# Performance work log

Measured on AMD Instinct MI355X. Metric: run time of the kernel, lower is better.

The kernel has to match this reference:

```python
import jax, jax.numpy as jnp
import numpy as np

N = 50000        # nodes
E = 1600000      # edges (avg degree 32)
N_IN = 128       # atomic embedding dim
N_F = 128        # filter dim
N_G = 50         # gaussian basis size for fij
CUTOFF = 5.0


def setup_inputs() -> dict:
    key = jax.random.key(0)
    ks = jax.random.split(key, 12)
    feat = jax.random.normal(ks[0], (N, N_IN), jnp.float32)
    fij = jax.random.uniform(ks[1], (E, N_G), dtype=jnp.float32)
    rij = jax.random.uniform(ks[2], (E,), dtype=jnp.float32) * CUTOFF
    src = jax.random.randint(ks[3], (E,), 0, N, dtype=jnp.int32)
    dst = jax.random.randint(ks[4], (E,), 0, N, dtype=jnp.int32)

    def w(k, shape, fan_in):
        return jax.random.normal(k, shape, jnp.float32) / np.float32(np.sqrt(fan_in))

    W_in2f = w(ks[5], (N_IN, N_F), N_IN)                 # Dense(n_in, n_filters, bias=False)
    Wf1 = w(ks[6], (N_G, N_F), N_G); bf1 = jnp.zeros((N_F,), jnp.float32)   # filter_network layer 1 (swish)
    Wf2 = w(ks[7], (N_F, N_F), N_F); bf2 = jnp.zeros((N_F,), jnp.float32)   # filter_network layer 2
    Wm1 = w(ks[8], (N_F, N_IN), N_F); bm1 = jnp.zeros((N_IN,), jnp.float32) # msg_transform layer 1 (swish)
    Wm2 = w(ks[9], (N_IN, N_IN), N_IN); bm2 = jnp.zeros((N_IN,), jnp.float32)
    return dict(feat=feat, fij=fij, rij=rij, src=src, dst=dst,
                W_in2f=W_in2f, Wf1=Wf1, bf1=bf1, Wf2=Wf2, bf2=bf2,
                Wm1=Wm1, bm1=bm1, Wm2=Wm2, bm2=bm2)


def _swish(x):
    return x * jax.nn.sigmoid(x)


def reference(feat, fij, rij, src, dst, W_in2f, Wf1, bf1, Wf2, bf2, Wm1, bm1, Wm2, bm2):
    # Cosine cutoff: 0.5*(cos(pi*r/rc)+1) for r < rc, else 0
    C = 0.5 * (jnp.cos(jnp.pi * rij / CUTOFF) + 1.0) * (rij < CUTOFF).astype(rij.dtype)
    # Edge filters: filter_network(fij) * C  -> [E, n_filters]
    he = (_swish(fij @ Wf1 + bf1) @ Wf2 + bf2) * C[:, None]
    # Node features projected: in2f(feat) -> [N, n_filters]
    hv = feat @ W_in2f
    # u_mul_e: gather source node feature, multiply by edge filter -> [E, n_filters]
    m = hv[src] * he
    # aggregator: sum messages at destination nodes -> [N, n_filters]
    agg = jax.ops.segment_sum(m, dst, num_segments=N)
    # msg_transform: Dense(swish) -> Dense
    return _swish(agg @ Wm1 + bm1) @ Wm2 + bm2
```

## Files before the change

### kernel.cpp

```cpp
#include <hip/hip_runtime.h>

#define N_NODES 50000
#define N_EDGES 1600000

typedef _Float16 f16x8 __attribute__((ext_vector_type(8)));
typedef float f32x4 __attribute__((ext_vector_type(4)));

__device__ __forceinline__ float fast_rcp(float v) {
#if __has_builtin(__builtin_amdgcn_rcpf)
    return __builtin_amdgcn_rcpf(v);
#else
    return __frcp_rn(v);
#endif
}

__global__ void prep_weights(const float* __restrict__ Wf1,
                             const float* __restrict__ Wf2,
                             const float* __restrict__ W_in2f,
                             const float* __restrict__ Wm1,
                             const float* __restrict__ Wm2,
                             _Float16* __restrict__ W1img,
                             _Float16* __restrict__ W2img,
                             _Float16* __restrict__ Wi2fimg,
                             _Float16* __restrict__ Wm1img,
                             _Float16* __restrict__ Wm2img) {
    int i = blockIdx.x * 256 + threadIdx.x;
    if (i < 8192) {
        int n = i >> 6, k = i & 63;
        float v = (k < 50) ? Wf1[k * 128 + n] : 0.0f;
        W1img[n * 64 + (((k >> 3) ^ (n & 7)) << 3) + (k & 7)] = (_Float16)v;
    }
    if (i < 16384) {
        int n = i >> 7, k = i & 127;
        int off = n * 128 + (((k >> 3) ^ (n & 7)) << 3) + (k & 7);
        int src = k * 128 + n;
        W2img[off]   = (_Float16)Wf2[src];
        Wi2fimg[off] = (_Float16)W_in2f[src];
        Wm1img[off]  = (_Float16)Wm1[src];
        Wm2img[off]  = (_Float16)Wm2[src];
    }
}

__global__ __launch_bounds__(512) void fused_hv_hist(
        const float* __restrict__ feat, const _Float16* __restrict__ Wi2fimg,
        _Float16* __restrict__ hvh,
        const int* __restrict__ dstv, int* __restrict__ cnt) {
    const int b = blockIdx.x;
    const int tid = threadIdx.x;
    if (b < 391) {
        const int lane = tid & 63, wv = tid >> 6;
        const int l15 = lane & 15, q = lane >> 4;
        const int row0 = b * 128;
        int ar = row0 + wv * 16 + l15;
        if (ar > N_NODES - 1) ar = N_NODES - 1;
        const float* arow = feat + (long)ar * 128;
        f16x8 a[4];
        #pragma unroll
        for (int ks = 0; ks < 4; ++ks) {
            const float* p = arow + ks * 32 + q * 8;
            float2 u0 = *(const float2*)(p + 0);
            float2 u1 = *(const float2*)(p + 2);
            float2 u2 = *(const float2*)(p + 4);
            float2 u3 = *(const float2*)(p + 6);
            a[ks][0] = (_Float16)u0.x; a[ks][1] = (_Float16)u0.y;
            a[ks][2] = (_Float16)u1.x; a[ks][3] = (_Float16)u1.y;
            a[ks][4] = (_Float16)u2.x; a[ks][5] = (_Float16)u2.y;
            a[ks][6] = (_Float16)u3.x; a[ks][7] = (_Float16)u3.y;
        }
        f32x4 acc[8];
        for (int nb = 0; nb < 8; ++nb) acc[nb] = (f32x4){0.f, 0.f, 0.f, 0.f};
        #pragma unroll
        for (int ks = 0; ks < 4; ++ks) {
            int c = ks * 4 + q;
            #pragma unroll
            for (int nb = 0; nb < 8; ++nb) {
                int n = nb * 16 + l15;
                f16x8 bf = *(const f16x8*)&Wi2fimg[n * 128 + ((c ^ (n & 7)) << 3)];
                acc[nb] = __builtin_amdgcn_mfma_f32_16x16x32_f16(a[ks], bf, acc[nb], 0, 0, 0);
            }
        }
        #pragma unroll
        for (int nb = 0; nb < 8; ++nb)
            #pragma unroll
            for (int r = 0; r < 4; ++r) {
                int orow = row0 + wv * 16 + q * 4 + r;
                if (orow < N_NODES)
                    hvh[(long)orow * 128 + nb * 16 + l15] = (_Float16)acc[nb][r];
            }
    } else {
        int e = (b - 391) * 512 + tid;
        if (e < N_EDGES) atomicAdd(&cnt[dstv[e]], 1);
    }
}

__global__ __launch_bounds__(1024) void scan_reduce(const int* __restrict__ cnt,
                                                    int* __restrict__ bsum) {
    __shared__ int ws[16];
    int tid = threadIdx.x, lane = tid & 63;
    int i = blockIdx.x * 1024 + tid;
    int x = (i < N_NODES) ? cnt[i] : 0;
    for (int o = 32; o > 0; o >>= 1) x += __shfl_down(x, o);
    if (lane == 0) ws[tid >> 6] = x;
    __syncthreads();
    if (tid == 0) {
        int s = 0;
        for (int w = 0; w < 16; ++w) s += ws[w];
        bsum[blockIdx.x] = s;
    }
}

__global__ void scan_top(int* __restrict__ bsum) {
    if (threadIdx.x == 0) {
        int s = 0;
        for (int b = 0; b < 49; ++b) { int v = bsum[b]; bsum[b] = s; s += v; }
    }
}

__global__ __launch_bounds__(1024) void scan_apply(int* __restrict__ cnt,
                                                   const int* __restrict__ bsum) {
    __shared__ int ws[16], wo[16];
    int tid = threadIdx.x, lane = tid & 63, wid = tid >> 6;
    int i = blockIdx.x * 1024 + tid;
    int x = (i < N_NODES) ? cnt[i] : 0;
    int incl = x;
    for (int o = 1; o < 64; o <<= 1) {
        int y = __shfl_up(incl, o);
        if (lane >= o) incl += y;
    }
    if (lane == 63) ws[wid] = incl;
    __syncthreads();
    if (tid == 0) {
        int s = 0;
        for (int w = 0; w < 16; ++w) { wo[w] = s; s += ws[w]; }
    }
    __syncthreads();
    if (i < N_NODES) cnt[i] = bsum[blockIdx.x] + wo[wid] + incl - x;
}

__global__ void scatter_kernel(const int* __restrict__ dstv,
                               const int* __restrict__ srcv,
                               const float* __restrict__ rij,
                               int* __restrict__ cursor,
                               int4* __restrict__ meta) {
    int e = blockIdx.x * 256 + threadIdx.x;
    if (e < N_EDGES) {
        int d = dstv[e];
        int pos = atomicAdd(&cursor[d], 1);
        meta[pos] = make_int4(e, srcv[e], d, __float_as_int(rij[e]));
    }
}

__global__ __launch_bounds__(512, 4) void edge_kernel(
        const float* __restrict__ fij, const _Float16* __restrict__ hvh,
        const _Float16* __restrict__ W1img, const _Float16* __restrict__ W2img,
        const float* __restrict__ bf1, const float* __restrict__ bf2,
        const int4* __restrict__ meta, float* __restrict__ agg) {
    __shared__ __align__(16) char smem[65536];
    __shared__ __align__(16) int4 sMeta[128];
    _Float16* sW1 = (_Float16*)smem;
    _Float16* sW2 = (_Float16*)(smem + 16384);
    _Float16* sT0 = (_Float16*)smem;
    _Float16* sT1 = (_Float16*)(smem + 49152);
    _Float16* sM  = (_Float16*)(smem + 16384);

    const int tid = threadIdx.x;
    const int lane = tid & 63;
    const int wv = tid >> 6;
    const int l15 = lane & 15;
    const int q = lane >> 4;
    const int e0 = blockIdx.x * 128;

    const int arow = wv * 16 + l15;
    const int eid = meta[e0 + arow].x;
    const float* frow = fij + (long)eid * 50;
    float2 p0 = *(const float2*)(frow + q * 8 + 0);
    float2 p1 = *(const float2*)(frow + q * 8 + 2);
    float2 p2 = *(const float2*)(frow + q * 8 + 4);
    float2 p3 = *(const float2*)(frow + q * 8 + 6);
    const int kb = 32 + q * 8;
    float2 z2 = make_float2(0.f, 0.f);
    float2 p4 = (kb + 1 < 50) ? *(const float2*)(frow + kb + 0) : z2;
    float2 p5 = (kb + 3 < 50) ? *(const float2*)(frow + kb + 2) : z2;
    float2 p6 = (kb + 5 < 50) ? *(const float2*)(frow + kb + 4) : z2;
    float2 p7 = (kb + 7 < 50) ? *(const float2*)(frow + kb + 6) : z2;
    f16x8 a0, a1;
    a0[0] = (_Float16)p0.x; a0[1] = (_Float16)p0.y;
    a0[2] = (_Float16)p1.x; a0[3] = (_Float16)p1.y;
    a0[4] = (_Float16)p2.x; a0[5] = (_Float16)p2.y;
    a0[6] = (_Float16)p3.x; a0[7] = (_Float16)p3.y;
    a1[0] = (_Float16)p4.x; a1[1] = (_Float16)p4.y;
    a1[2] = (_Float16)p5.x; a1[3] = (_Float16)p5.y;
    a1[4] = (_Float16)p6.x; a1[5] = (_Float16)p6.y;
    a1[6] = (_Float16)p7.x; a1[7] = (_Float16)p7.y;

    if (tid < 128) sMeta[tid] = meta[e0 + tid];
    {
        const float4* s1 = (const float4*)W1img;
        float4* d1 = (float4*)sW1;
        d1[tid] = s1[tid]; d1[tid + 512] = s1[tid + 512];
        const float4* s2 = (const float4*)W2img;
        float4* d2 = (float4*)sW2;
        for (int t = 0; t < 4; ++t) d2[tid + 512 * t] = s2[tid + 512 * t];
    }
    float b1v[8], b2v[8];
    for (int nb = 0; nb < 8; ++nb) {
        b1v[nb] = bf1[nb * 16 + l15];
        b2v[nb] = bf2[nb * 16 + l15];
    }
    __syncthreads();

    const int col2 = tid & 63;
    const int rseg0 = (tid >> 6) * 16;
    unsigned int pf[16];
    #pragma unroll
    for (int i = 0; i < 16; ++i) {
        long srcn = sMeta[rseg0 + i].y;
        pf[i] = *(const unsigned int*)(hvh + srcn * 128 + col2 * 2);
    }

    f32x4 acc[8];
    for (int nb = 0; nb < 8; ++nb) acc[nb] = (f32x4){0.f, 0.f, 0.f, 0.f};
    {
        f16x8 b[8];
        for (int nb = 0; nb < 8; ++nb) {
            int n = nb * 16 + l15;
            b[nb] = *(const f16x8*)&sW1[n * 64 + ((q ^ (n & 7)) << 3)];
        }
        for (int nb = 0; nb < 8; ++nb)
            acc[nb] = __builtin_amdgcn_mfma_f32_16x16x32_f16(a0, b[nb], acc[nb], 0, 0, 0);
        for (int nb = 0; nb < 8; ++nb) {
            int n = nb * 16 + l15;
            b[nb] = *(const f16x8*)&sW1[n * 64 + (((4 + q) ^ (n & 7)) << 3)];
        }
        for (int nb = 0; nb < 8; ++nb)
            acc[nb] = __builtin_amdgcn_mfma_f32_16x16x32_f16(a1, b[nb], acc[nb], 0, 0, 0);
    }
    __syncthreads();

    for (int nb = 0; nb < 8; ++nb)
        for (int r = 0; r < 4; ++r) {
            float x = acc[nb][r] + b1v[nb];
            float tt = x * fast_rcp(1.0f + __expf(-x));
            int row = wv * 16 + q * 4 + r;
            int col = nb * 16 + l15;
            _Float16* base = (row < 64) ? sT0 + row * 128 : sT1 + (row - 64) * 128;
            base[(((col >> 3) ^ (row & 7)) << 3) + (col & 7)] = (_Float16)tt;
        }
    __syncthreads();

    for (int nb = 0; nb < 8; ++nb) acc[nb] = (f32x4){0.f, 0.f, 0.f, 0.f};
    {
        const int row = wv * 16 + l15;
        const _Float16* abase = (row < 64) ? sT0 + row * 128 : sT1 + (row - 64) * 128;
        for (int ks = 0; ks < 4; ++ks) {
            int c = ks * 4 + q;
            f16x8 a = *(const f16x8*)&abase[(c ^ (row & 7)) << 3];
            for (int nb = 0; nb < 8; ++nb) {
                int n = nb * 16 + l15;
                f16x8 b = *(const f16x8*)&sW2[n * 128 + ((c ^ (n & 7)) << 3)];
                acc[nb] = __builtin_amdgcn_mfma_f32_16x16x32_f16(a, b, acc[nb], 0, 0, 0);
            }
        }
    }
    __syncthreads();

    for (int r = 0; r < 4; ++r) {
        int row = wv * 16 + q * 4 + r;
        float rv = __int_as_float(sMeta[row].w);
        float Cr = (rv < 5.0f) ? 0.5f * (__cosf(0.6283185307179586f * rv) + 1.0f) : 0.0f;
        for (int nb = 0; nb < 8; ++nb) {
            int col = nb * 16 + l15;
            sM[row * 132 + col] = (_Float16)((acc[nb][r] + b2v[nb]) * Cr);
        }
    }
    __syncthreads();

    {
        float run0 = 0.0f, run1 = 0.0f;
        int cur = sMeta[rseg0].z;
        #pragma unroll
        for (int i = 0; i < 16; ++i) {
            int r = rseg0 + i;
            int d = sMeta[r].z;
            if (d != cur) {
                atomicAdd(&agg[cur * 128 + col2 * 2], run0);
                atomicAdd(&agg[cur * 128 + col2 * 2 + 1], run1);
                run0 = 0.0f; run1 = 0.0f; cur = d;
            }
            union { unsigned int u; _Float16 h[2]; } hv2; hv2.u = pf[i];
            union { unsigned int u; _Float16 h[2]; } m2;
            m2.u = *(const unsigned int*)&sM[r * 132 + col2 * 2];
            run0 += (float)hv2.h[0] * (float)m2.h[0];
            run1 += (float)hv2.h[1] * (float)m2.h[1];
        }
        atomicAdd(&agg[cur * 128 + col2 * 2], run0);
        atomicAdd(&agg[cur * 128 + col2 * 2 + 1], run1);
    }
}

__global__ __launch_bounds__(512) void out_kernel(const float* __restrict__ agg,
                                                  const _Float16* __restrict__ Wm1img,
                                                  const float* __restrict__ bm1,
                                                  const _Float16* __restrict__ Wm2img,
                                                  const float* __restrict__ bm2,
                                                  float* __restrict__ out) {
    __shared__ __align__(16) _Float16 sT[128 * 128];
    const int tid = threadIdx.x, lane = tid & 63, wv = tid >> 6;
    const int l15 = lane & 15, q = lane >> 4;
    const int row0 = blockIdx.x * 128;
    int ar = row0 + wv * 16 + l15;
    if (ar > N_NODES - 1) ar = N_NODES - 1;
    const float* arow = agg + (long)ar * 128;
    f16x8 a[4];
    #pragma unroll
    for (int ks = 0; ks < 4; ++ks) {
        const float* p = arow + ks * 32 + q * 8;
        float2 u0 = *(const float2*)(p + 0);
        float2 u1 = *(const float2*)(p + 2);
        float2 u2 = *(const float2*)(p + 4);
        float2 u3 = *(const float2*)(p + 6);
        a[ks][0] = (_Float16)u0.x; a[ks][1] = (_Float16)u0.y;
        a[ks][2] = (_Float16)u1.x; a[ks][3] = (_Float16)u1.y;
        a[ks][4] = (_Float16)u2.x; a[ks][5] = (_Float16)u2.y;
        a[ks][6] = (_Float16)u3.x; a[ks][7] = (_Float16)u3.y;
    }
    float b1v[8], b2v[8];
    for (int nb = 0; nb < 8; ++nb) {
        b1v[nb] = bm1[nb * 16 + l15];
        b2v[nb] = bm2[nb * 16 + l15];
    }
    f32x4 acc[8];
    for (int nb = 0; nb < 8; ++nb) acc[nb] = (f32x4){0.f, 0.f, 0.f, 0.f};
    #pragma unroll
    for (int ks = 0; ks < 4; ++ks) {
        int c = ks * 4 + q;
        #pragma unroll
        for (int nb = 0; nb < 8; ++nb) {
            int n = nb * 16 + l15;
            f16x8 bf = *(const f16x8*)&Wm1img[n * 128 + ((c ^ (n & 7)) << 3)];
            acc[nb] = __builtin_amdgcn_mfma_f32_16x16x32_f16(a[ks], bf, acc[nb], 0, 0, 0);
        }
    }
    #pragma unroll
    for (int nb = 0; nb < 8; ++nb)
        #pragma unroll
        for (int r = 0; r < 4; ++r) {
            float x = acc[nb][r] + b1v[nb];
            float tt = x * fast_rcp(1.0f + __expf(-x));
            int row = wv * 16 + q * 4 + r;
            int col = nb * 16 + l15;
            sT[row * 128 + (((col >> 3) ^ (row & 7)) << 3) + (col & 7)] = (_Float16)tt;
        }
    __syncthreads();
    for (int nb = 0; nb < 8; ++nb) acc[nb] = (f32x4){0.f, 0.f, 0.f, 0.f};
    {
        const int rowA = wv * 16 + l15;
        const _Float16* abase = &sT[rowA * 128];
        #pragma unroll
        for (int ks = 0; ks < 4; ++ks) {
            int c = ks * 4 + q;
            f16x8 a2 = *(const f16x8*)&abase[(c ^ (rowA & 7)) << 3];
            #pragma unroll
            for (int nb = 0; nb < 8; ++nb) {
                int n = nb * 16 + l15;
                f16x8 bf = *(const f16x8*)&Wm2img[n * 128 + ((c ^ (n & 7)) << 3)];
                acc[nb] = __builtin_amdgcn_mfma_f32_16x16x32_f16(a2, bf, acc[nb], 0, 0, 0);
            }
        }
    }
    #pragma unroll
    for (int nb = 0; nb < 8; ++nb)
        #pragma unroll
        for (int r = 0; r < 4; ++r) {
            int orow = row0 + wv * 16 + q * 4 + r;
            if (orow < N_NODES)
                out[(long)orow * 128 + nb * 16 + l15] = acc[nb][r] + b2v[nb];
        }
}

extern "C" void kernel_launch(void* const* d_in, const int* in_sizes, int n_in,
                              void* d_out, int out_size, void* d_ws, size_t ws_size,
                              hipStream_t stream) {
    const float* feat   = (const float*)d_in[0];
    const float* fij    = (const float*)d_in[1];
    const float* rij    = (const float*)d_in[2];
    const int*   srcv   = (const int*)d_in[3];
    const int*   dstv   = (const int*)d_in[4];
    const float* W_in2f = (const float*)d_in[5];
    const float* Wf1    = (const float*)d_in[6];
    const float* bf1    = (const float*)d_in[7];
    const float* Wf2    = (const float*)d_in[8];
    const float* bf2    = (const float*)d_in[9];
    const float* Wm1    = (const float*)d_in[10];
    const float* bm1    = (const float*)d_in[11];
    const float* Wm2    = (const float*)d_in[12];
    const float* bm2    = (const float*)d_in[13];
    float* out = (float*)d_out;

    char* ws = (char*)d_ws;
    float*    agg     = (float*)ws;
    _Float16* hvh     = (_Float16*)(ws + 25600000);
    int4*     meta    = (int4*)(ws + 38400000);
    int*      cnt     = (int*)(ws + 64000000);
    int*      bsum    = (int*)(ws + 64200000);
    _Float16* W1img   = (_Float16*)(ws + 64200704);
    _Float16* W2img   = (_Float16*)(ws + 64217088);
    _Float16* Wi2fimg = (_Float16*)(ws + 64249856);
    _Float16* Wm1img  = (_Float16*)(ws + 64282624);
    _Float16* Wm2img  = (_Float16*)(ws + 64315392);

    hipMemsetAsync(agg, 0, (size_t)N_NODES * 128 * sizeof(float), stream);
    hipMemsetAsync(cnt, 0, (size_t)N_NODES * sizeof(int), stream);
    prep_weights<<<64, 256, 0, stream>>>(Wf1, Wf2, W_in2f, Wm1, Wm2,
                                         W1img, W2img, Wi2fimg, Wm1img, Wm2img);
    fused_hv_hist<<<391 + 3125, 512, 0, stream>>>(feat, Wi2fimg, hvh, dstv, cnt);
    scan_reduce<<<49, 1024, 0, stream>>>(cnt, bsum);
    scan_top<<<1, 64, 0, stream>>>(bsum);
    scan_apply<<<49, 1024, 0, stream>>>(cnt, bsum);
    scatter_kernel<<<(N_EDGES + 255) / 256, 256, 0, stream>>>(dstv, srcv, rij, cnt, meta);
    edge_kernel<<<12500, 512, 0, stream>>>(fij, hvh, W1img, W2img, bf1, bf2, meta, agg);
    out_kernel<<<391, 512, 0, stream>>>(agg, Wm1img, bm1, Wm2img, bm2, out);
}
```

Before: 871.7 us.

## Read filter weights from global, make edge kernel wave-local and barrier-free

Weight tiles W1/W2 are no longer staged into shared memory. MFMA B fragments are loaded straight from the global weight images, relying on cache hits. Because each wave only touches its own 16 rows, the intermediate and message buffers are merged into one 32KB swizzled shared array and all block-wide barriers after setup are removed. Launch bounds are raised to request more resident blocks. The cost is much more cache traffic for weight fragments, and register pressure from the tighter occupancy target could cause spills.

```diff
diff --git a/kernel.cpp b/kernel.cpp
--- a/kernel.cpp
+++ b/kernel.cpp
@@ -150,18 +150,13 @@
     }
 }
 
-__global__ __launch_bounds__(512, 4) void edge_kernel(
+__global__ __launch_bounds__(512, 8) void edge_kernel(
         const float* __restrict__ fij, const _Float16* __restrict__ hvh,
         const _Float16* __restrict__ W1img, const _Float16* __restrict__ W2img,
         const float* __restrict__ bf1, const float* __restrict__ bf2,
         const int4* __restrict__ meta, float* __restrict__ agg) {
-    __shared__ __align__(16) char smem[65536];
+    __shared__ __align__(16) _Float16 sTM[128 * 128];
     __shared__ __align__(16) int4 sMeta[128];
-    _Float16* sW1 = (_Float16*)smem;
-    _Float16* sW2 = (_Float16*)(smem + 16384);
-    _Float16* sT0 = (_Float16*)smem;
-    _Float16* sT1 = (_Float16*)(smem + 49152);
-    _Float16* sM  = (_Float16*)(smem + 16384);
 
     const int tid = threadIdx.x;
     const int lane = tid & 63;
@@ -194,14 +189,6 @@
     a1[6] = (_Float16)p7.x; a1[7] = (_Float16)p7.y;
 
     if (tid < 128) sMeta[tid] = meta[e0 + tid];
-    {
-        const float4* s1 = (const float4*)W1img;
-        float4* d1 = (float4*)sW1;
-        d1[tid] = s1[tid]; d1[tid + 512] = s1[tid + 512];
-        const float4* s2 = (const float4*)W2img;
-        float4* d2 = (float4*)sW2;
-        for (int t = 0; t < 4; ++t) d2[tid + 512 * t] = s2[tid + 512 * t];
-    }
     float b1v[8], b2v[8];
     for (int nb = 0; nb < 8; ++nb) {
         b1v[nb] = bf1[nb * 16 + l15];
@@ -209,8 +196,23 @@
     }
     __syncthreads();
 
+    f32x4 acc[8];
+    for (int nb = 0; nb < 8; ++nb) acc[nb] = (f32x4){0.f, 0.f, 0.f, 0.f};
+    #pragma unroll
+    for (int nb = 0; nb < 8; ++nb) {
+        int n = nb * 16 + l15;
+        f16x8 b = *(const f16x8*)&W1img[n * 64 + ((q ^ (n & 7)) << 3)];
+        acc[nb] = __builtin_amdgcn_mfma_f32_16x16x32_f16(a0, b, acc[nb], 0, 0, 0);
+    }
+    #pragma unroll
+    for (int nb = 0; nb < 8; ++nb) {
+        int n = nb * 16 + l15;
+        f16x8 b = *(const f16x8*)&W1img[n * 64 + (((4 + q) ^ (n & 7)) << 3)];
+        acc[nb] = __builtin_amdgcn_mfma_f32_16x16x32_f16(a1, b, acc[nb], 0, 0, 0);
+    }
+
     const int col2 = tid & 63;
-    const int rseg0 = (tid >> 6) * 16;
+    const int rseg0 = wv * 16;
     unsigned int pf[16];
     #pragma unroll
     for (int i = 0; i < 16; ++i) {
@@ -218,62 +220,46 @@
         pf[i] = *(const unsigned int*)(hvh + srcn * 128 + col2 * 2);
     }
 
-    f32x4 acc[8];
-    for (int nb = 0; nb < 8; ++nb) acc[nb] = (f32x4){0.f, 0.f, 0.f, 0.f};
-    {
-        f16x8 b[8];
-        for (int nb = 0; nb < 8; ++nb) {
-            int n = nb * 16 + l15;
-            b[nb] = *(const f16x8*)&sW1[n * 64 + ((q ^ (n & 7)) << 3)];
-        }
-        for (int nb = 0; nb < 8; ++nb)
-            acc[nb] = __builtin_amdgcn_mfma_f32_16x16x32_f16(a0, b[nb], acc[nb], 0, 0, 0);
-        for (int nb = 0; nb < 8; ++nb) {
-            int n = nb * 16 + l15;
-            b[nb] = *(const f16x8*)&sW1[n * 64 + (((4 + q) ^ (n & 7)) << 3)];
-        }
-        for (int nb = 0; nb < 8; ++nb)
-            acc[nb] = __builtin_amdgcn_mfma_f32_16x16x32_f16(a1, b[nb], acc[nb], 0, 0, 0);
-    }
-    __syncthreads();
-
+    #pragma unroll
     for (int nb = 0; nb < 8; ++nb)
+        #pragma unroll
         for (int r = 0; r < 4; ++r) {
             float x = acc[nb][r] + b1v[nb];
             float tt = x * fast_rcp(1.0f + __expf(-x));
             int row = wv * 16 + q * 4 + r;
             int col = nb * 16 + l15;
-            _Float16* base = (row < 64) ? sT0 + row * 128 : sT1 + (row - 64) * 128;
-            base[(((col >> 3) ^ (row & 7)) << 3) + (col & 7)] = (_Float16)tt;
-        }
-    __syncthreads();
+            sTM[row * 128 + (((col >> 3) ^ (row & 7)) << 3) + (col & 7)] = (_Float16)tt;
+        }
 
     for (int nb = 0; nb < 8; ++nb) acc[nb] = (f32x4){0.f, 0.f, 0.f, 0.f};
     {
         const int row = wv * 16 + l15;
-        const _Float16* abase = (row < 64) ? sT0 + row * 128 : sT1 + (row - 64) * 128;
+        const _Float16* abase = &sTM[row * 128];
+        #pragma unroll
         for (int ks = 0; ks < 4; ++ks) {
             int c = ks * 4 + q;
             f16x8 a = *(const f16x8*)&abase[(c ^ (row & 7)) << 3];
+            #pragma unroll
             for (int nb = 0; nb < 8; ++nb) {
                 int n = nb * 16 + l15;
-                f16x8 b = *(const f16x8*)&sW2[n * 128 + ((c ^ (n & 7)) << 3)];
+                f16x8 b = *(const f16x8*)&W2img[n * 128 + ((c ^ (n & 7)) << 3)];
                 acc[nb] = __builtin_amdgcn_mfma_f32_16x16x32_f16(a, b, acc[nb], 0, 0, 0);
             }
         }
     }
-    __syncthreads();
-
+
+    #pragma unroll
     for (int r = 0; r < 4; ++r) {
         int row = wv * 16 + q * 4 + r;
         float rv = __int_as_float(sMeta[row].w);
         float Cr = (rv < 5.0f) ? 0.5f * (__cosf(0.6283185307179586f * rv) + 1.0f) : 0.0f;
+        #pragma unroll
         for (int nb = 0; nb < 8; ++nb) {
             int col = nb * 16 + l15;
-            sM[row * 132 + col] = (_Float16)((acc[nb][r] + b2v[nb]) * Cr);
-        }
-    }
-    __syncthreads();
+            sTM[row * 128 + (((col >> 3) ^ (row & 7)) << 3) + (col & 7)] =
+                (_Float16)((acc[nb][r] + b2v[nb]) * Cr);
+        }
+    }
 
     {
         float run0 = 0.0f, run1 = 0.0f;
@@ -289,7 +275,8 @@
             }
             union { unsigned int u; _Float16 h[2]; } hv2; hv2.u = pf[i];
             union { unsigned int u; _Float16 h[2]; } m2;
-            m2.u = *(const unsigned int*)&sM[r * 132 + col2 * 2];
+            m2.u = *(const unsigned int*)
+                &sTM[r * 128 + ((((col2 >> 2) ^ (r & 7)) << 3) + ((col2 & 3) << 1))];
             run0 += (float)hv2.h[0] * (float)m2.h[0];
             run1 += (float)hv2.h[1] * (float)m2.h[1];
         }
```

Result: slower. 1.574 ms (+80.6%).
